# Kernel tuning notes

Hardware: AMD Instinct MI355X
Metric: run time of the kernel (lower is better)

## Reference

```python
import jax, jax.numpy as jnp
import numpy as np

F, N, D, K = 32, 4096, 64, 512
COMMITMENT_COST = 0.25


def setup_inputs() -> dict:
    key = jax.random.key(0)
    k1, k2 = jax.random.split(key)
    inputs = jax.random.normal(k1, (F, N, D), dtype=jnp.float32)
    # GlorotUniform on weight shape [F, D, K]
    limit = float(np.sqrt(6.0 / (D + K)))
    w = jax.random.uniform(k2, (F, D, K), dtype=jnp.float32, minval=-limit, maxval=limit)
    return {"inputs": inputs, "w": w}


def reference(inputs, w):
    # inputs: [F, N, D], w: [F, D, K]
    distances = (
        jnp.sum(inputs ** 2, axis=2, keepdims=True)
        - 2.0 * jnp.einsum('fnd,fdk->fnk', inputs, w)
        + jnp.sum(w ** 2, axis=1, keepdims=True)
    )
    enc_idx = jnp.argmin(distances, axis=2)  # [F, N]
    w_t = jnp.swapaxes(w, 1, 2)  # [F, K, D]
    quantized = jnp.take_along_axis(w_t, enc_idx[:, :, None], axis=1)  # [F, N, D]
    e_latent_loss = jnp.mean((jax.lax.stop_gradient(quantized) - inputs) ** 2)
    q_latent_loss = jnp.mean((quantized - jax.lax.stop_gradient(inputs)) ** 2)
    loss = q_latent_loss + COMMITMENT_COST * e_latent_loss
    # straight-through estimator
    output = inputs + jax.lax.stop_gradient(quantized - inputs)
    return output, loss
```

## Files before the change

### kernel.cpp

```cpp
#include <hip/hip_runtime.h>
#include <math.h>

#define NF 32
#define NN 4096
#define ND 64
#define NK 512

#define LOSS_SCALE (1.25f / (float)(NF * NN * ND))
#define TAU 3e-4f

typedef short bf16x8 __attribute__((ext_vector_type(8)));
typedef float f32x4 __attribute__((ext_vector_type(4)));

static __device__ __forceinline__ unsigned short f2bf_rne(float f) {
    unsigned int u = __float_as_uint(f);
    u += 0x7FFFu + ((u >> 16) & 1u);
    return (unsigned short)(u >> 16);
}
static __device__ __forceinline__ float bf2f(unsigned short h) {
    return __uint_as_float(((unsigned int)h) << 16);
}

static __device__ __forceinline__ void gload_lds16(const void* g, void* l) {
    __builtin_amdgcn_global_load_lds(
        (const __attribute__((address_space(1))) unsigned int*)g,
        (__attribute__((address_space(3))) unsigned int*)l, 16, 0, 0);
}

__global__ __launch_bounds__(256)
void vq_prep_w(const float* __restrict__ w, float* __restrict__ wt,
               unsigned short* __restrict__ wh, unsigned short* __restrict__ wl,
               float* __restrict__ w2h, float* __restrict__ loss_slot) {
    __shared__ float lds[64 * 65];
    const int t  = threadIdx.x;
    const int f  = blockIdx.x >> 3;
    const int k0 = (blockIdx.x & 7) * 64;
    const float* __restrict__ wf = w + (size_t)f * ND * NK;

    if (blockIdx.x == 0 && t == 0) *loss_slot = 0.0f;

    {
        const int d = t >> 2, qq = t & 3;
#pragma unroll
        for (int i = 0; i < 4; ++i) {
            const int c4 = qq + i * 4;
            const float4 v = *(const float4*)(wf + (size_t)d * NK + k0 + c4 * 4);
            lds[d * 65 + c4 * 4 + 0] = v.x;
            lds[d * 65 + c4 * 4 + 1] = v.y;
            lds[d * 65 + c4 * 4 + 2] = v.z;
            lds[d * 65 + c4 * 4 + 3] = v.w;
        }
    }
    __syncthreads();

    const int k = t >> 2, p = t & 3;
    float v[16];
    float s = 0.0f;
#pragma unroll
    for (int j = 0; j < 16; ++j) {
        v[j] = lds[(p * 16 + j) * 65 + k];
        s = fmaf(v[j], v[j], s);
    }
    s += __shfl_xor(s, 1, 64);
    s += __shfl_xor(s, 2, 64);
    if (p == 0) w2h[f * NK + k0 + k] = 0.5f * s;

    const size_t rowo = ((size_t)f * NK + k0 + k) * ND + p * 16;
    unsigned short hh[16], ll[16];
#pragma unroll
    for (int j = 0; j < 16; ++j) {
        hh[j] = f2bf_rne(v[j]);
        ll[j] = f2bf_rne(v[j] - bf2f(hh[j]));
    }
#pragma unroll
    for (int i = 0; i < 4; ++i) {
        *(float4*)(wt + rowo + i * 4) =
            make_float4(v[i*4+0], v[i*4+1], v[i*4+2], v[i*4+3]);
        *(ushort4*)(wh + rowo + i * 4) =
            make_ushort4(hh[i*4+0], hh[i*4+1], hh[i*4+2], hh[i*4+3]);
        *(ushort4*)(wl + rowo + i * 4) =
            make_ushort4(ll[i*4+0], ll[i*4+1], ll[i*4+2], ll[i*4+3]);
    }
}

__global__ __launch_bounds__(256, 4)
void vq_argmin(const float* __restrict__ x_in,
               const unsigned short* __restrict__ wh,
               const unsigned short* __restrict__ wl,
               const float* __restrict__ wt,
               const float* __restrict__ w2h,
               float* __restrict__ out,
               float* __restrict__ loss_slot) {
    const int b    = blockIdx.x;
    const int j    = b >> 3;
    const int f    = (b & 7) * 4 + (j & 3);
    const int xt   = j >> 2;
    const int tid  = threadIdx.x;
    const int wave = tid >> 6;
    const int lane = tid & 63;
    const int lc   = lane & 15;
    const int q    = lane >> 4;
    const int n0   = xt * 128 + wave * 32;
    const int g0b  = f * NN + xt * 128;

    __shared__ float w2s[NK];
    __shared__ __align__(16) unsigned short bstage[2][4096];
    __shared__ unsigned int lds_key[128];
    __shared__ unsigned char lds_flag[128];

    for (int t = tid; t < NK; t += 256) w2s[t] = w2h[f * NK + t];

    bf16x8 ah[2][2], al[2][2];
    const float* __restrict__ xbase = x_in + ((size_t)f * NN + n0 + lc) * ND;
#pragma unroll
    for (int mt = 0; mt < 2; ++mt) {
#pragma unroll
        for (int s = 0; s < 2; ++s) {
            const float* p = xbase + mt * 16 * ND + s * 32 + q * 8;
            float4 u0 = *(const float4*)(p);
            float4 u1 = *(const float4*)(p + 4);
            float xv[8] = {-u0.x, -u0.y, -u0.z, -u0.w, -u1.x, -u1.y, -u1.z, -u1.w};
            bf16x8 hh, ll;
#pragma unroll
            for (int jj = 0; jj < 8; ++jj) {
                unsigned short hb = f2bf_rne(xv[jj]);
                unsigned short lb = f2bf_rne(xv[jj] - bf2f(hb));
                hh[jj] = (short)hb;
                ll[jj] = (short)lb;
            }
            ah[mt][s] = hh;
            al[mt][s] = ll;
        }
    }

    const unsigned short* __restrict__ whf = wh + (size_t)f * NK * ND;
    const unsigned short* __restrict__ wlf = wl + (size_t)f * NK * ND;

    float m1[8], m2[8], kmin[8];
#pragma unroll
    for (int ri = 0; ri < 8; ++ri) { m1[ri] = INFINITY; m2[ri] = INFINITY; kmin[ri] = INFINITY; }

#define STAGE(st, pb) do {                                                  \
    _Pragma("unroll")                                                       \
    for (int rep = 0; rep < 2; ++rep) {                                     \
        const int c  = wave * 2 + rep;                                      \
        const int tl = c >> 2;                                              \
        const int sg = (c >> 1) & 1;                                        \
        const unsigned short* src = ((c & 1) ? wlf : whf) +                 \
            (size_t)((st) * 32 + tl * 16 + lc) * ND + q * 8 + sg * 32;      \
        gload_lds16(src, &bstage[pb][c * 512]);                             \
    }                                                                       \
} while (0)

    STAGE(0, 0);

    for (int st = 0; st < 16; ++st) {
        __syncthreads();
        if (st < 15) STAGE(st + 1, (st + 1) & 1);
        const unsigned short* __restrict__ bb = &bstage[st & 1][0];

#pragma unroll
        for (int tl = 0; tl < 2; ++tl) {
            const int col = st * 32 + tl * 16 + lc;
            bf16x8 bh0 = *(const bf16x8*)(bb + (tl * 4 + 0) * 512 + lane * 8);
            bf16x8 bl0 = *(const bf16x8*)(bb + (tl * 4 + 1) * 512 + lane * 8);
            bf16x8 bh1 = *(const bf16x8*)(bb + (tl * 4 + 2) * 512 + lane * 8);
            bf16x8 bl1 = *(const bf16x8*)(bb + (tl * 4 + 3) * 512 + lane * 8);
            const float w2 = w2s[col];
#pragma unroll
            for (int mt = 0; mt < 2; ++mt) {
                f32x4 c = {w2, w2, w2, w2};
                c = __builtin_amdgcn_mfma_f32_16x16x32_bf16(ah[mt][0], bh0, c, 0, 0, 0);
                c = __builtin_amdgcn_mfma_f32_16x16x32_bf16(ah[mt][1], bh1, c, 0, 0, 0);
                c = __builtin_amdgcn_mfma_f32_16x16x32_bf16(ah[mt][0], bl0, c, 0, 0, 0);
                c = __builtin_amdgcn_mfma_f32_16x16x32_bf16(ah[mt][1], bl1, c, 0, 0, 0);
                c = __builtin_amdgcn_mfma_f32_16x16x32_bf16(al[mt][0], bh0, c, 0, 0, 0);
                c = __builtin_amdgcn_mfma_f32_16x16x32_bf16(al[mt][1], bh1, c, 0, 0, 0);
#pragma unroll
                for (int r = 0; r < 4; ++r) {
                    const int ri = mt * 4 + r;
                    const float sc = c[r];
                    const float key = __uint_as_float(
                        (__float_as_uint(sc) & 0xFFFFFE00u) | (unsigned int)col);
                    kmin[ri] = fminf(kmin[ri], key);
                    m2[ri] = __builtin_amdgcn_fmed3f(sc, m1[ri], m2[ri]);
                    m1[ri] = fminf(sc, m1[ri]);
                }
            }
        }
    }

#pragma unroll
    for (int ri = 0; ri < 8; ++ri) {
        float a1 = m1[ri], a2 = m2[ri], ak = kmin[ri];
#pragma unroll
        for (int off = 1; off < 16; off <<= 1) {
            const float b1 = __shfl_xor(a1, off, 64);
            const float b2 = __shfl_xor(a2, off, 64);
            const float bk = __shfl_xor(ak, off, 64);
            a2 = fminf(fminf(a2, b2), fmaxf(a1, b1));
            a1 = fminf(a1, b1);
            ak = fminf(ak, bk);
        }
        m1[ri] = a1; m2[ri] = a2; kmin[ri] = ak;
    }

    if (lc == 0) {
#pragma unroll
        for (int mt = 0; mt < 2; ++mt) {
#pragma unroll
            for (int r = 0; r < 4; ++r) {
                const int ri = mt * 4 + r;
                const int lr = wave * 32 + mt * 16 + q * 4 + r;
                lds_key[lr]  = __float_as_uint(kmin[ri]) & 0x1FFu;
                lds_flag[lr] = (m2[ri] - m1[ri] < TAU) ? 1 : 0;
            }
        }
    }
    __syncthreads();

    {
        const int lr32 = wave * 32 + (lane & 31);
        const int fl = (lane < 32) ? lds_flag[lr32] : 0;
        unsigned long long mm = __ballot(fl != 0);
        const float* __restrict__ wtf = wt + (size_t)f * NK * ND;
        while (mm) {
            const int r = __ffsll(mm) - 1;
            mm &= mm - 1;
            const int grow = g0b + wave * 32 + r;
            const float* __restrict__ xr = x_in + (size_t)grow * ND;
            unsigned long long best = 0xFFFFFFFFFFFFFFFFULL;
#pragma unroll 1
            for (int jj = 0; jj < 8; ++jj) {
                const int col = jj * 64 + lane;
                const float* __restrict__ wr = wtf + (size_t)col * ND;
                float t = w2s[col];
#pragma unroll
                for (int d = 0; d < ND; d += 4) {
                    float4 xv = *(const float4*)(xr + d);
                    float4 wv = *(const float4*)(wr + d);
                    t = fmaf(-xv.x, wv.x, t);
                    t = fmaf(-xv.y, wv.y, t);
                    t = fmaf(-xv.z, wv.z, t);
                    t = fmaf(-xv.w, wv.w, t);
                }
                unsigned int u = __float_as_uint(t);
                u ^= (unsigned int)((int)u >> 31) | 0x80000000u;
                const unsigned long long key =
                    ((unsigned long long)u << 32) | (unsigned int)col;
                best = key < best ? key : best;
            }
#pragma unroll
            for (int off = 32; off > 0; off >>= 1) {
                const unsigned long long o = __shfl_xor(best, off, 64);
                best = o < best ? o : best;
            }
            if (lane == 0) lds_key[wave * 32 + r] = (unsigned int)(best & 0x1FFu);
        }
    }
    __syncthreads();

    {
        const int row_l = tid >> 1;
        const int part  = tid & 1;
        const int grow  = g0b + row_l;
        const unsigned int k = lds_key[row_l];
        const float* __restrict__ q32 = wt + ((size_t)f * NK + k) * ND + part * 32;
        const float* __restrict__ x32 = x_in + (size_t)grow * ND + part * 32;
        float* __restrict__ o32       = out + (size_t)grow * ND + part * 32;

        float lsum = 0.0f;
#pragma unroll
        for (int jj = 0; jj < 8; ++jj) {
            float4 qv = *(const float4*)(q32 + 4 * jj);
            float4 xv = *(const float4*)(x32 + 4 * jj);
            const float dx0 = qv.x - xv.x;
            const float dx1 = qv.y - xv.y;
            const float dx2 = qv.z - xv.z;
            const float dx3 = qv.w - xv.w;
            lsum = fmaf(dx0, dx0, lsum);
            lsum = fmaf(dx1, dx1, lsum);
            lsum = fmaf(dx2, dx2, lsum);
            lsum = fmaf(dx3, dx3, lsum);
            *(float4*)(o32 + 4 * jj) = qv;
        }

#pragma unroll
        for (int off = 32; off > 0; off >>= 1) {
            lsum += __shfl_down(lsum, off, 64);
        }
        __shared__ float wsum[4];
        if ((tid & 63) == 0) wsum[tid >> 6] = lsum;
        __syncthreads();
        if (tid == 0) {
            atomicAdd(loss_slot,
                      (wsum[0] + wsum[1] + wsum[2] + wsum[3]) * LOSS_SCALE);
        }
    }
}

extern "C" void kernel_launch(void* const* d_in, const int* in_sizes, int n_in,
                              void* d_out, int out_size, void* d_ws, size_t ws_size,
                              hipStream_t stream) {
    const float* x_in = (const float*)d_in[0];
    const float* w    = (const float*)d_in[1];
    float* out        = (float*)d_out;

    float* wt  = (float*)d_ws;
    float* w2h = wt + (size_t)NF * NK * ND;
    unsigned short* wh = (unsigned short*)(w2h + NF * NK);
    unsigned short* wl = wh + (size_t)NF * NK * ND;

    float* loss_slot = out + (size_t)NF * NN * ND;

    vq_prep_w<<<NF * 8, 256, 0, stream>>>(w, wt, wh, wl, w2h, loss_slot);

    vq_argmin<<<NF * NN / 128, 256, 0, stream>>>(x_in, wh, wl, wt, w2h,
                                                 out, loss_slot);
}
```

Before: 148.1 us.

## Fuse codebook prep into argmin kernel with per-feature spin barrier

Removes the separate weight-preparation kernel. Each argmin block now transposes, splits to bf16 hi/lo and computes half-norms for a 16-column slice of its feature's codebook. The 32 blocks of a feature then synchronise through an atomic counter spin barrier before the main loop. The per-row min tracking is changed to keep the two smallest packed keys instead of separate score and index minima, with a wider rescue threshold. The loss is now accumulated in workspace and written by the last block, which adds a memset launch and relies on all 32 blocks per feature being co-resident to avoid deadlock.

```diff
diff --git a/kernel.cpp b/kernel.cpp
--- a/kernel.cpp
+++ b/kernel.cpp
@@ -7,7 +7,7 @@
 #define NK 512
 
 #define LOSS_SCALE (1.25f / (float)(NF * NN * ND))
-#define TAU 3e-4f
+#define RESCUE_TAU 5.5e-4f
 
 typedef short bf16x8 __attribute__((ext_vector_type(8)));
 typedef float f32x4 __attribute__((ext_vector_type(4)));
@@ -27,70 +27,12 @@
         (__attribute__((address_space(3))) unsigned int*)l, 16, 0, 0);
 }
 
-__global__ __launch_bounds__(256)
-void vq_prep_w(const float* __restrict__ w, float* __restrict__ wt,
-               unsigned short* __restrict__ wh, unsigned short* __restrict__ wl,
-               float* __restrict__ w2h, float* __restrict__ loss_slot) {
-    __shared__ float lds[64 * 65];
-    const int t  = threadIdx.x;
-    const int f  = blockIdx.x >> 3;
-    const int k0 = (blockIdx.x & 7) * 64;
-    const float* __restrict__ wf = w + (size_t)f * ND * NK;
-
-    if (blockIdx.x == 0 && t == 0) *loss_slot = 0.0f;
-
-    {
-        const int d = t >> 2, qq = t & 3;
-#pragma unroll
-        for (int i = 0; i < 4; ++i) {
-            const int c4 = qq + i * 4;
-            const float4 v = *(const float4*)(wf + (size_t)d * NK + k0 + c4 * 4);
-            lds[d * 65 + c4 * 4 + 0] = v.x;
-            lds[d * 65 + c4 * 4 + 1] = v.y;
-            lds[d * 65 + c4 * 4 + 2] = v.z;
-            lds[d * 65 + c4 * 4 + 3] = v.w;
-        }
-    }
-    __syncthreads();
-
-    const int k = t >> 2, p = t & 3;
-    float v[16];
-    float s = 0.0f;
-#pragma unroll
-    for (int j = 0; j < 16; ++j) {
-        v[j] = lds[(p * 16 + j) * 65 + k];
-        s = fmaf(v[j], v[j], s);
-    }
-    s += __shfl_xor(s, 1, 64);
-    s += __shfl_xor(s, 2, 64);
-    if (p == 0) w2h[f * NK + k0 + k] = 0.5f * s;
-
-    const size_t rowo = ((size_t)f * NK + k0 + k) * ND + p * 16;
-    unsigned short hh[16], ll[16];
-#pragma unroll
-    for (int j = 0; j < 16; ++j) {
-        hh[j] = f2bf_rne(v[j]);
-        ll[j] = f2bf_rne(v[j] - bf2f(hh[j]));
-    }
-#pragma unroll
-    for (int i = 0; i < 4; ++i) {
-        *(float4*)(wt + rowo + i * 4) =
-            make_float4(v[i*4+0], v[i*4+1], v[i*4+2], v[i*4+3]);
-        *(ushort4*)(wh + rowo + i * 4) =
-            make_ushort4(hh[i*4+0], hh[i*4+1], hh[i*4+2], hh[i*4+3]);
-        *(ushort4*)(wl + rowo + i * 4) =
-            make_ushort4(ll[i*4+0], ll[i*4+1], ll[i*4+2], ll[i*4+3]);
-    }
-}
-
 __global__ __launch_bounds__(256, 4)
-void vq_argmin(const float* __restrict__ x_in,
-               const unsigned short* __restrict__ wh,
-               const unsigned short* __restrict__ wl,
-               const float* __restrict__ wt,
-               const float* __restrict__ w2h,
-               float* __restrict__ out,
-               float* __restrict__ loss_slot) {
+void vq_fused(const float* __restrict__ x_in, const float* __restrict__ w,
+              float* __restrict__ wt, unsigned short* __restrict__ wh,
+              unsigned short* __restrict__ wl, float* __restrict__ w2h,
+              unsigned int* __restrict__ syncws,
+              float* __restrict__ out, float* __restrict__ loss_slot) {
     const int b    = blockIdx.x;
     const int j    = b >> 3;
     const int f    = (b & 7) * 4 + (j & 3);
@@ -107,8 +49,7 @@
     __shared__ __align__(16) unsigned short bstage[2][4096];
     __shared__ unsigned int lds_key[128];
     __shared__ unsigned char lds_flag[128];
-
-    for (int t = tid; t < NK; t += 256) w2s[t] = w2h[f * NK + t];
+    __shared__ float wsum[4];
 
     bf16x8 ah[2][2], al[2][2];
     const float* __restrict__ xbase = x_in + ((size_t)f * NN + n0 + lc) * ND;
@@ -133,12 +74,63 @@
         }
     }
 
+    {
+        float* __restrict__ tl = (float*)&bstage[0][0];
+        const int k0 = xt * 16;
+        const float* __restrict__ wf = w + (size_t)f * ND * NK;
+        const int d = tid >> 2, c4 = tid & 3;
+        const float4 v4 = *(const float4*)(wf + (size_t)d * NK + k0 + c4 * 4);
+        tl[d * 17 + c4 * 4 + 0] = v4.x;
+        tl[d * 17 + c4 * 4 + 1] = v4.y;
+        tl[d * 17 + c4 * 4 + 2] = v4.z;
+        tl[d * 17 + c4 * 4 + 3] = v4.w;
+        __syncthreads();
+
+        const int k = tid >> 4, p = tid & 15;
+        float v[4];
+        float s = 0.0f;
+#pragma unroll
+        for (int j4 = 0; j4 < 4; ++j4) {
+            v[j4] = tl[(p * 4 + j4) * 17 + k];
+            s = fmaf(v[j4], v[j4], s);
+        }
+        s += __shfl_xor(s, 1, 64);
+        s += __shfl_xor(s, 2, 64);
+        s += __shfl_xor(s, 4, 64);
+        s += __shfl_xor(s, 8, 64);
+        if (p == 0) w2h[f * NK + k0 + k] = 0.5f * s;
+
+        const size_t rowo = ((size_t)f * NK + k0 + k) * ND + p * 4;
+        unsigned short hh[4], ll[4];
+#pragma unroll
+        for (int j4 = 0; j4 < 4; ++j4) {
+            hh[j4] = f2bf_rne(v[j4]);
+            ll[j4] = f2bf_rne(v[j4] - bf2f(hh[j4]));
+        }
+        *(float4*)(wt + rowo)  = make_float4(v[0], v[1], v[2], v[3]);
+        *(ushort4*)(wh + rowo) = make_ushort4(hh[0], hh[1], hh[2], hh[3]);
+        *(ushort4*)(wl + rowo) = make_ushort4(ll[0], ll[1], ll[2], ll[3]);
+    }
+
+    __threadfence();
+    __syncthreads();
+    if (tid == 0) {
+        atomicAdd(&syncws[f], 1u);
+        while (atomicAdd(&syncws[f], 0u) < 32u) {
+            __builtin_amdgcn_s_sleep(2);
+        }
+    }
+    __syncthreads();
+    __threadfence();
+
+    for (int t = tid; t < NK; t += 256) w2s[t] = w2h[f * NK + t];
+
     const unsigned short* __restrict__ whf = wh + (size_t)f * NK * ND;
     const unsigned short* __restrict__ wlf = wl + (size_t)f * NK * ND;
 
-    float m1[8], m2[8], kmin[8];
-#pragma unroll
-    for (int ri = 0; ri < 8; ++ri) { m1[ri] = INFINITY; m2[ri] = INFINITY; kmin[ri] = INFINITY; }
+    float k1[8], k2[8];
+#pragma unroll
+    for (int ri = 0; ri < 8; ++ri) { k1[ri] = INFINITY; k2[ri] = INFINITY; }
 
 #define STAGE(st, pb) do {                                                  \
     _Pragma("unroll")                                                       \
@@ -179,12 +171,10 @@
 #pragma unroll
                 for (int r = 0; r < 4; ++r) {
                     const int ri = mt * 4 + r;
-                    const float sc = c[r];
                     const float key = __uint_as_float(
-                        (__float_as_uint(sc) & 0xFFFFFE00u) | (unsigned int)col);
-                    kmin[ri] = fminf(kmin[ri], key);
-                    m2[ri] = __builtin_amdgcn_fmed3f(sc, m1[ri], m2[ri]);
-                    m1[ri] = fminf(sc, m1[ri]);
+                        (__float_as_uint(c[r]) & 0xFFFFFE00u) | (unsigned int)col);
+                    k2[ri] = __builtin_amdgcn_fmed3f(key, k1[ri], k2[ri]);
+                    k1[ri] = fminf(key, k1[ri]);
                 }
             }
         }
@@ -192,17 +182,15 @@
 
 #pragma unroll
     for (int ri = 0; ri < 8; ++ri) {
-        float a1 = m1[ri], a2 = m2[ri], ak = kmin[ri];
+        float a1 = k1[ri], a2 = k2[ri];
 #pragma unroll
         for (int off = 1; off < 16; off <<= 1) {
             const float b1 = __shfl_xor(a1, off, 64);
             const float b2 = __shfl_xor(a2, off, 64);
-            const float bk = __shfl_xor(ak, off, 64);
             a2 = fminf(fminf(a2, b2), fmaxf(a1, b1));
             a1 = fminf(a1, b1);
-            ak = fminf(ak, bk);
-        }
-        m1[ri] = a1; m2[ri] = a2; kmin[ri] = ak;
+        }
+        k1[ri] = a1; k2[ri] = a2;
     }
 
     if (lc == 0) {
@@ -212,8 +200,12 @@
             for (int r = 0; r < 4; ++r) {
                 const int ri = mt * 4 + r;
                 const int lr = wave * 32 + mt * 16 + q * 4 + r;
-                lds_key[lr]  = __float_as_uint(kmin[ri]) & 0x1FFu;
-                lds_flag[lr] = (m2[ri] - m1[ri] < TAU) ? 1 : 0;
+                const unsigned int u1 = __float_as_uint(k1[ri]);
+                const unsigned int u2 = __float_as_uint(k2[ri]);
+                lds_key[lr] = u1 & 0x1FFu;
+                const float s1 = __uint_as_float(u1 & 0xFFFFFE00u);
+                const float s2 = __uint_as_float(u2 & 0xFFFFFE00u);
+                lds_flag[lr] = (s2 - s1 < RESCUE_TAU) ? 1 : 0;
             }
         }
     }
@@ -289,12 +281,18 @@
         for (int off = 32; off > 0; off >>= 1) {
             lsum += __shfl_down(lsum, off, 64);
         }
-        __shared__ float wsum[4];
         if ((tid & 63) == 0) wsum[tid >> 6] = lsum;
         __syncthreads();
         if (tid == 0) {
-            atomicAdd(loss_slot,
+            atomicAdd((float*)&syncws[33],
                       (wsum[0] + wsum[1] + wsum[2] + wsum[3]) * LOSS_SCALE);
+            __threadfence();
+            const unsigned int old = atomicAdd(&syncws[32], 1u);
+            if (old == 1023u) {
+                __threadfence();
+                const float total = atomicAdd((float*)&syncws[33], 0.0f);
+                *loss_slot = total;
+            }
         }
     }
 }
@@ -306,15 +304,16 @@
     const float* w    = (const float*)d_in[1];
     float* out        = (float*)d_out;
 
-    float* wt  = (float*)d_ws;
+    unsigned int* syncws = (unsigned int*)d_ws;
+    float* wt  = (float*)((char*)d_ws + 256);
     float* w2h = wt + (size_t)NF * NK * ND;
     unsigned short* wh = (unsigned short*)(w2h + NF * NK);
     unsigned short* wl = wh + (size_t)NF * NK * ND;
 
     float* loss_slot = out + (size_t)NF * NN * ND;
 
-    vq_prep_w<<<NF * 8, 256, 0, stream>>>(w, wt, wh, wl, w2h, loss_slot);
-
-    vq_argmin<<<NF * NN / 128, 256, 0, stream>>>(x_in, wh, wl, wt, w2h,
-                                                 out, loss_slot);
-}
+    hipMemsetAsync(d_ws, 0, 256, stream);
+
+    vq_fused<<<NF * NN / 128, 256, 0, stream>>>(x_in, w, wt, wh, wl, w2h,
+                                                syncws, out, loss_slot);
+}
```

New measurement: 397.1 us. +168.1%, slower.
